# Optimization experiments

Measured on AMD Instinct MI355X. Metric: run time of the kernel, lower is better.

Reference implementation:

```python
import jax, jax.numpy as jnp
import numpy as np

HEADS = 20
HEAD_DIM = 64
NUM_IP = 20          # num_content_tokens (4) + num_style_tokens (16)
FU_SCALE = 0.5
STYLE_SCALE = 1.0
SCALE = 1.0 / np.sqrt(HEAD_DIM).astype(np.float32)


def setup_inputs() -> dict:
    key = jax.random.key(0)
    ks = jax.random.split(key, 9)
    B, S, H, C = 4, 4096, 1280, 2048
    T = 77 + NUM_IP  # text tokens + ip tokens
    w = 0.02
    return {
        "hidden_states": jax.random.normal(ks[0], (B, S, H), jnp.float32),
        "encoder_hidden_states": jax.random.normal(ks[1], (B, T, C), jnp.float32),
        "Wq": jax.random.normal(ks[2], (H, H), jnp.float32) * w,
        "Wk": jax.random.normal(ks[3], (H, C), jnp.float32) * w,
        "Wv": jax.random.normal(ks[4], (H, C), jnp.float32) * w,
        "Wk_ip": jax.random.normal(ks[5], (H, C), jnp.float32) * w,
        "Wv_ip": jax.random.normal(ks[6], (H, C), jnp.float32) * w,
        "Wo": jax.random.normal(ks[7], (H, H), jnp.float32) * w,
        "bo": jnp.zeros((H,), jnp.float32),
    }


def _to_heads(x):
    # [B, T, H] -> [B, heads, T, head_dim]
    B, T, _ = x.shape
    return x.reshape(B, T, HEADS, HEAD_DIM).transpose(0, 2, 1, 3)


def _blend(p):
    # cross-batch prob fusion: rows 1<-0, 3<-2 (CFG pairs)
    p = p.at[1].set(FU_SCALE * p[1] + (1.0 - FU_SCALE) * p[0])
    p = p.at[3].set(FU_SCALE * p[3] + (1.0 - FU_SCALE) * p[2])
    return p


def reference(hidden_states, encoder_hidden_states, Wq, Wk, Wv, Wk_ip, Wv_ip, Wo, bo):
    B, S, H = hidden_states.shape
    text = encoder_hidden_states[:, :-NUM_IP, :]   # [B, 77, C]
    ip = encoder_hidden_states[:, -NUM_IP:, :]     # [B, 20, C]

    q = _to_heads(hidden_states @ Wq.T)            # [B, h, S, d]
    k = _to_heads(text @ Wk.T)                     # [B, h, 77, d]
    v = _to_heads(text @ Wv.T)

    # fuAttn branch: explicit probs, blended across batch, then PV matmul
    probs = jax.nn.softmax(jnp.einsum('bhqd,bhkd->bhqk', q, k) * SCALE, axis=-1)
    probs = _blend(probs)
    raw = jnp.einsum('bhqk,bhkd->bhqd', probs, v)
    raw = raw.transpose(0, 2, 1, 3).reshape(B, S, H)

    # IP-adapter style cross-attention (fuIPAttn branch)
    ip_k = _to_heads(ip @ Wk_ip.T)                 # [B, h, 20, d]
    ip_v = _to_heads(ip @ Wv_ip.T)
    ip_probs = jax.nn.softmax(jnp.einsum('bhqd,bhkd->bhqk', q, ip_k) * SCALE, axis=-1)
    ip_probs = _blend(ip_probs)
    ip_hs = jnp.einsum('bhqk,bhkd->bhqd', ip_probs, ip_v)
    ip_hs = ip_hs.transpose(0, 2, 1, 3).reshape(B, S, H)

    hs = raw + STYLE_SCALE * ip_hs
    # batch rows 0 and 2 keep raw (text-only) attention output
    hs = hs.at[0].set(raw[0]).at[2].set(raw[2])

    # to_out[0] linear (bias) + to_out[1] dropout (identity at inference)
    return hs @ Wo.T + bo
```

## Files before the change

kernel.cpp:

```cpp
#include <hip/hip_runtime.h>
#include <cstdint>

typedef float floatx4 __attribute__((ext_vector_type(4)));
typedef __bf16 bf16x8 __attribute__((ext_vector_type(8)));

typedef const __attribute__((address_space(1))) void* gas_cvp;
typedef __attribute__((address_space(3))) void* las_vp;

__device__ __forceinline__ float bflo(unsigned int u) {
    return __builtin_bit_cast(float, u << 16);
}
__device__ __forceinline__ float bfhi(unsigned int u) {
    return __builtin_bit_cast(float, u & 0xffff0000u);
}
__device__ __forceinline__ unsigned short f2bf(float f) {
    unsigned int u = __builtin_bit_cast(unsigned int, f);
    u += 0x7fffu + ((u >> 16) & 1u);
    return (unsigned short)(u >> 16);
}
__device__ __forceinline__ bf16x8 ld8(const unsigned short* p) {
    return __builtin_bit_cast(bf16x8, *(const uint4*)p);
}
__device__ __forceinline__ floatx4 mfma32(bf16x8 a, bf16x8 b, floatx4 c) {
    return __builtin_amdgcn_mfma_f32_16x16x32_bf16(a, b, c, 0, 0, 0);
}
__device__ __forceinline__ void load_lds16(const void* g, void* l) {
    __builtin_amdgcn_global_load_lds(
        (gas_cvp)(unsigned long long)g,
        (las_vp)(unsigned int)(unsigned long long)l,
        16, 0, 0);
}

__global__ void cvt_f32_bf16(const float* __restrict__ in,
                             unsigned short* __restrict__ out, int n4) {
    int i = blockIdx.x * 256 + threadIdx.x;
    if (i < n4) {
        float4 v = ((const float4*)in)[i];
        ushort4 o;
        o.x = f2bf(v.x); o.y = f2bf(v.y); o.z = f2bf(v.z); o.w = f2bf(v.w);
        ((ushort4*)out)[i] = o;
    }
}

struct CvtJob { const float* src; unsigned short* dst; int n4; };
struct CvtJobs { CvtJob j[6]; };

__global__ void cvt_multi(CvtJobs jobs) {
    CvtJob jb = jobs.j[blockIdx.y];
    int i = blockIdx.x * 256 + threadIdx.x;
    if (i < jb.n4) {
        float4 v = ((const float4*)jb.src)[i];
        ushort4 o;
        o.x = f2bf(v.x); o.y = f2bf(v.y); o.z = f2bf(v.z); o.w = f2bf(v.w);
        ((ushort4*)jb.dst)[i] = o;
    }
}

__global__ void cvt_ehs(const float* __restrict__ ehs,
                        unsigned short* __restrict__ text,
                        unsigned short* __restrict__ ip) {
    int i = blockIdx.x * 256 + threadIdx.x;
    if (i < 384 * 512) {
        int r = i >> 9, c = i & 511;
        int b = r / 96, t = r - b * 96;
        ushort4 o = {0, 0, 0, 0};
        if (t < 77) {
            float4 v = *(const float4*)&ehs[((size_t)(b * 97 + t)) * 2048 + c * 4];
            o.x = f2bf(v.x); o.y = f2bf(v.y); o.z = f2bf(v.z); o.w = f2bf(v.w);
        }
        ((ushort4*)text)[i] = o;
    } else {
        int i2 = i - 384 * 512;
        if (i2 < 128 * 512) {
            int r = i2 >> 9, c = i2 & 511;
            int b = r >> 5, t = r & 31;
            ushort4 o = {0, 0, 0, 0};
            if (t < 20) {
                float4 v = *(const float4*)&ehs[((size_t)(b * 97 + 77 + t)) * 2048 + c * 4];
                o.x = f2bf(v.x); o.y = f2bf(v.y); o.z = f2bf(v.z); o.w = f2bf(v.w);
            }
            ((ushort4*)ip)[i2] = o;
        }
    }
}

struct GJob {
    const unsigned short* A;
    const unsigned short* B;
    void* C;
    int M, K;
    int Bn;
    int nt;
    int ldc;
    int bstart;
};
struct GArgs { GJob j[5]; };

template <bool F32OUT>
__global__ __launch_bounds__(512, 2) void gemm256(GArgs args,
                                                  const float* __restrict__ bias) {
    const int tid = threadIdx.x;
    int jid = 0;
#pragma unroll
    for (int t = 1; t < 5; ++t)
        if ((int)blockIdx.x >= args.j[t].bstart) jid = t;
    const GJob jb = args.j[jid];
    const int K = jb.K;
    int b = (int)blockIdx.x - jb.bstart;
    {
        const int mt = (jb.M + 255) >> 8;
        const int nblk = mt * jb.nt;
        if ((nblk & 7) == 0) b = (b & 7) * (nblk >> 3) + (b >> 3);
    }
    const int by = b / jb.nt, bx = b - by * jb.nt;

    __shared__ unsigned short ldsA[32768];
    __shared__ unsigned short ldsB[32768];

    const int srow   = ((tid >> 7) << 4) + ((tid >> 2) & 15);
    const int schunk = ((tid & 3) << 4) ^ (((tid >> 2) & 6) << 3);
    const int scol   = (((tid >> 6) & 1) << 5) + (schunk >> 1);

    const int Mloc = jb.M, BnL = jb.Bn;

    const unsigned short* pA[2][2];
    const unsigned short* pB[2][2];
    unsigned short* dA[2][2];
    unsigned short* dB[2][2];
#pragma unroll
    for (int h = 0; h < 2; ++h)
#pragma unroll
        for (int j = 0; j < 2; ++j) {
            const int r = h * 128 + j * 64 + srow;
            int ra = by * 256 + r;  ra = (ra < Mloc) ? ra : (Mloc - 1);
            int rb2 = bx * 256 + r; rb2 = (rb2 < BnL) ? rb2 : (BnL - 1);
            pA[h][j] = jb.A + (size_t)ra * K + scol;
            pB[h][j] = jb.B + (size_t)rb2 * K + scol;
            dA[h][j] = &ldsA[h * 8192 + j * 4096 + tid * 8];
            dB[h][j] = &ldsB[h * 8192 + j * 4096 + tid * 8];
        }

    const int lane = tid & 63, fr = lane & 15, g = lane >> 4;
    const int w = tid >> 6, wr = w & 1, wc = w >> 1;
    const int rb   = fr * 32 + ((g * 8) ^ ((fr & 6) << 2));
    const int aoff = wr * 8192 + rb;
    const int boff = (wc >> 1) * 8192 + (wc & 1) * 4096 + rb;

    floatx4 acc[8][4] = {};

    const int KT = K >> 6;

#pragma unroll
    for (int h = 0; h < 2; ++h)
#pragma unroll
        for (int j = 0; j < 2; ++j) {
            load_lds16(pA[h][j], dA[h][j]);
            load_lds16(pB[h][j], dB[h][j]);
        }
    asm volatile("s_waitcnt vmcnt(0)" ::: "memory");
    __builtin_amdgcn_s_barrier();

    for (int u = 0; u < KT; ++u) {
        const int pb = (u & 1) << 14;
        const int qb = pb ^ 16384;
        const int k1 = (u + 1 < KT) ? (u + 1) : (KT - 1);

#pragma unroll
        for (int h = 0; h < 2; ++h)
#pragma unroll
            for (int j = 0; j < 2; ++j) {
                load_lds16(pA[h][j] + (size_t)k1 * 64, dA[h][j] + qb);
                load_lds16(pB[h][j] + (size_t)k1 * 64, dB[h][j] + qb);
            }
        __builtin_amdgcn_sched_barrier(0);

#pragma unroll
        for (int kk = 0; kk < 2; ++kk) {
            bf16x8 af[8], bfr[4];
#pragma unroll
            for (int mi = 0; mi < 8; ++mi)
                af[mi] = *(const bf16x8*)&ldsA[pb + aoff + (mi * 2 + kk) * 512];
#pragma unroll
            for (int nf = 0; nf < 4; ++nf)
                bfr[nf] = *(const bf16x8*)&ldsB[pb + boff + (nf * 2 + kk) * 512];
            __builtin_amdgcn_s_setprio(1);
#pragma unroll
            for (int mi = 0; mi < 8; ++mi)
#pragma unroll
                for (int nf = 0; nf < 4; ++nf)
                    acc[mi][nf] = mfma32(af[mi], bfr[nf], acc[mi][nf]);
            __builtin_amdgcn_s_setprio(0);
        }

        asm volatile("s_waitcnt vmcnt(0)" ::: "memory");
        __builtin_amdgcn_s_barrier();
    }

    const int colBase = bx * 256 + wc * 64;
    const int rowBase = by * 256 + wr * 128;
    const int ldc = jb.ldc;
    float bv[4] = {};
    if (F32OUT) {
#pragma unroll
        for (int nf = 0; nf < 4; ++nf) bv[nf] = bias[colBase + nf * 16 + fr];
    }
#pragma unroll
    for (int mi = 0; mi < 8; ++mi) {
#pragma unroll
        for (int nf = 0; nf < 4; ++nf) {
            const int col  = colBase + nf * 16 + fr;
            const int row0 = rowBase + mi * 16 + g * 4;
#pragma unroll
            for (int r = 0; r < 4; ++r) {
                const int row = row0 + r;
                if (row < Mloc) {
                    float v = acc[mi][nf][r];
                    if (F32OUT)
                        ((float*)jb.C)[(size_t)row * ldc + col] = v + bv[nf];
                    else
                        ((unsigned short*)jb.C)[(size_t)row * ldc + col] = f2bf(v);
                }
            }
        }
    }
}

#define NT 77
#define NI 20

__global__ __launch_bounds__(256, 4) void attn_mfma(
    const unsigned short* __restrict__ q,
    const unsigned short* __restrict__ kt,
    const unsigned short* __restrict__ vtT,
    const unsigned short* __restrict__ kip,
    const unsigned short* __restrict__ ipT,
    unsigned short* __restrict__ outp)
{
    const int tid = threadIdx.x;
    const int qt = blockIdx.x;
    const int h  = blockIdx.y;
    const int pz = blockIdx.z;
    const int b0 = 2 * pz;
    const int lane  = tid & 63;
    const int w     = tid >> 6;
    const int bi    = w >> 1;
    const int strip = (w & 1) * 16;
    const int fr = lane & 15;
    const int g  = lane >> 4;

    __shared__ unsigned short sP[2][32][104];

    for (int i = tid; i < 2 * 32 * 24; i += 256) {
        int b = i / (32 * 24); int rem = i % (32 * 24);
        sP[b][rem / 24][80 + rem % 24] = 0;
    }

    const size_t qbase = ((size_t)((b0 + bi) * 4096 + qt * 32 + strip + fr)) * 1280 + h * 64;
    bf16x8 aq0 = ld8(&q[qbase + g * 8]);
    bf16x8 aq1 = ld8(&q[qbase + 32 + g * 8]);

    floatx4 sc[5] = {};
#pragma unroll
    for (int t = 0; t < 5; t++) {
        int key = t * 16 + fr;
        const size_t kb = ((size_t)((b0 + bi) * 96 + key)) * 1280 + h * 64;
        sc[t] = mfma32(aq0, ld8(&kt[kb + g * 8]), sc[t]);
        sc[t] = mfma32(aq1, ld8(&kt[kb + 32 + g * 8]), sc[t]);
    }

#pragma unroll
    for (int r = 0; r < 4; r++) {
        float m = -1e30f;
#pragma unroll
        for (int t = 0; t < 5; t++) {
            float v = sc[t][r] * 0.125f;
            if (t == 4 && fr >= 13) v = -1e30f;
            sc[t][r] = v;
            m = fmaxf(m, v);
        }
        m = fmaxf(m, __shfl_xor(m, 1));
        m = fmaxf(m, __shfl_xor(m, 2));
        m = fmaxf(m, __shfl_xor(m, 4));
        m = fmaxf(m, __shfl_xor(m, 8));
        float sum = 0.f;
#pragma unroll
        for (int t = 0; t < 5; t++) {
            float e = __expf(sc[t][r] - m);
            sc[t][r] = e;
            sum += e;
        }
        sum += __shfl_xor(sum, 1);
        sum += __shfl_xor(sum, 2);
        sum += __shfl_xor(sum, 4);
        sum += __shfl_xor(sum, 8);
        float inv = 1.f / sum;
#pragma unroll
        for (int t = 0; t < 5; t++)
            sP[bi][strip + g * 4 + r][t * 16 + fr] = f2bf(sc[t][r] * inv);
    }
    __syncthreads();

    {
        unsigned int* p0 = (unsigned int*)&sP[0][0][0];
        unsigned int* p1 = (unsigned int*)&sP[1][0][0];
        for (int i = tid; i < 32 * 104 / 2; i += 256) {
            unsigned int a = p0[i], b = p1[i];
            unsigned short r0 = f2bf(0.5f * (bflo(a) + bflo(b)));
            unsigned short r1 = f2bf(0.5f * (bfhi(a) + bfhi(b)));
            p1[i] = (unsigned int)r0 | ((unsigned int)r1 << 16);
        }
    }
    __syncthreads();

    floatx4 accO[4] = {};
    {
        const unsigned short* prow = &sP[bi][strip + fr][0];
        bf16x8 pa0 = ld8(prow + g * 8);
        bf16x8 pa1 = ld8(prow + 32 + g * 8);
        bf16x8 pa2 = ld8(prow + 64 + g * 8);
        const int vcol = (b0 + bi) * 96;
#pragma unroll
        for (int dt = 0; dt < 4; dt++) {
            const unsigned short* vrow = &vtT[(size_t)(h * 64 + dt * 16 + fr) * 512 + vcol];
            accO[dt] = mfma32(pa0, ld8(vrow + g * 8), accO[dt]);
            accO[dt] = mfma32(pa1, ld8(vrow + 32 + g * 8), accO[dt]);
            accO[dt] = mfma32(pa2, ld8(vrow + 64 + g * 8), accO[dt]);
        }
    }

    floatx4 si[2] = {};
#pragma unroll
    for (int t = 0; t < 2; t++) {
        int key = t * 16 + fr;
        const size_t kb = ((size_t)((b0 + bi) * 32 + key)) * 1280 + h * 64;
        si[t] = mfma32(aq0, ld8(&kip[kb + g * 8]), si[t]);
        si[t] = mfma32(aq1, ld8(&kip[kb + 32 + g * 8]), si[t]);
    }
#pragma unroll
    for (int r = 0; r < 4; r++) {
        float v0 = si[0][r] * 0.125f;
        float v1 = (fr >= 4) ? -1e30f : si[1][r] * 0.125f;
        float m = fmaxf(v0, v1);
        m = fmaxf(m, __shfl_xor(m, 1));
        m = fmaxf(m, __shfl_xor(m, 2));
        m = fmaxf(m, __shfl_xor(m, 4));
        m = fmaxf(m, __shfl_xor(m, 8));
        float e0 = __expf(v0 - m), e1 = __expf(v1 - m);
        float s = e0 + e1;
        s += __shfl_xor(s, 1);
        s += __shfl_xor(s, 2);
        s += __shfl_xor(s, 4);
        s += __shfl_xor(s, 8);
        float inv = 1.f / s;
        si[0][r] = e0 * inv;
        si[1][r] = e1 * inv;
    }
    __syncthreads();

#pragma unroll
    for (int r = 0; r < 4; r++) {
        sP[bi][strip + g * 4 + r][fr]      = f2bf(si[0][r]);
        sP[bi][strip + g * 4 + r][16 + fr] = f2bf(si[1][r]);
    }
    __syncthreads();

    for (int i = tid; i < 32 * 16; i += 256) {
        int r = i >> 4, kk = i & 15;
        unsigned int* p0 = (unsigned int*)&sP[0][r][0];
        unsigned int* p1 = (unsigned int*)&sP[1][r][0];
        unsigned int a = p0[kk], b = p1[kk];
        unsigned short r0 = f2bf(0.5f * (bflo(a) + bflo(b)));
        unsigned short r1 = f2bf(0.5f * (bfhi(a) + bfhi(b)));
        p1[kk] = (unsigned int)r0 | ((unsigned int)r1 << 16);
    }
    __syncthreads();

    if (bi == 1) {
        const unsigned short* prow = &sP[1][strip + fr][0];
        bf16x8 pip = ld8(prow + g * 8);
        const int icol = (b0 + 1) * 32;
#pragma unroll
        for (int dt = 0; dt < 4; dt++)
            accO[dt] = mfma32(pip,
                              ld8(&ipT[(size_t)(h * 64 + dt * 16 + fr) * 256 + icol + g * 8]),
                              accO[dt]);
    }

    const size_t orow0 = (size_t)((b0 + bi) * 4096 + qt * 32 + strip);
#pragma unroll
    for (int dt = 0; dt < 4; dt++) {
        int col = h * 64 + dt * 16 + fr;
#pragma unroll
        for (int r = 0; r < 4; r++)
            outp[(orow0 + g * 4 + r) * 1280 + col] = f2bf(accO[dt][r]);
    }
}

extern "C" void kernel_launch(void* const* d_in, const int* in_sizes, int n_in,
                              void* d_out, int out_size, void* d_ws, size_t ws_size,
                              hipStream_t stream) {
    const float* hs   = (const float*)d_in[0];
    const float* ehs  = (const float*)d_in[1];
    const float* Wq   = (const float*)d_in[2];
    const float* Wk   = (const float*)d_in[3];
    const float* Wv   = (const float*)d_in[4];
    const float* Wkip = (const float*)d_in[5];
    const float* Wvip = (const float*)d_in[6];
    const float* Wo   = (const float*)d_in[7];
    const float* bo   = (const float*)d_in[8];

    char* w = (char*)d_ws;
    size_t off = 0;
    auto alloc = [&](size_t bytes) {
        char* pp = w + off;
        off += (bytes + 255) & ~(size_t)255;
        return pp;
    };
    unsigned short* hs_bf   = (unsigned short*)alloc(16384ull * 1280 * 2);
    unsigned short* q_bf    = (unsigned short*)alloc(16384ull * 1280 * 2);
    unsigned short* at_bf   = (unsigned short*)alloc(16384ull * 1280 * 2);
    unsigned short* text_pad= (unsigned short*)alloc(384ull * 2048 * 2);
    unsigned short* ip_pad  = (unsigned short*)alloc(128ull * 2048 * 2);
    unsigned short* Wq_bf   = (unsigned short*)alloc(1280ull * 1280 * 2);
    unsigned short* Wk_bf   = (unsigned short*)alloc(1280ull * 2048 * 2);
    unsigned short* Wv_bf   = (unsigned short*)alloc(1280ull * 2048 * 2);
    unsigned short* Wkip_bf = (unsigned short*)alloc(1280ull * 2048 * 2);
    unsigned short* Wvip_bf = (unsigned short*)alloc(1280ull * 2048 * 2);
    unsigned short* Wo_bf   = (unsigned short*)alloc(1280ull * 1280 * 2);
    unsigned short* kt  = (unsigned short*)alloc(384ull * 1280 * 2);
    unsigned short* vtT = (unsigned short*)alloc(1280ull * 512 * 2);
    unsigned short* kip = (unsigned short*)alloc(128ull * 1280 * 2);
    unsigned short* ipT = (unsigned short*)alloc(1280ull * 256 * 2);

    cvt_f32_bf16<<<dim3(20480, 1, 1), 256, 0, stream>>>(hs, hs_bf, 16384 * 1280 / 4);

    cvt_ehs<<<dim3(1024, 1, 1), 256, 0, stream>>>(ehs, text_pad, ip_pad);

    CvtJobs cj{};
    cj.j[0] = CvtJob{Wq,   Wq_bf,   1280 * 1280 / 4};
    cj.j[1] = CvtJob{Wk,   Wk_bf,   1280 * 2048 / 4};
    cj.j[2] = CvtJob{Wv,   Wv_bf,   1280 * 2048 / 4};
    cj.j[3] = CvtJob{Wkip, Wkip_bf, 1280 * 2048 / 4};
    cj.j[4] = CvtJob{Wvip, Wvip_bf, 1280 * 2048 / 4};
    cj.j[5] = CvtJob{Wo,   Wo_bf,   1280 * 1280 / 4};
    cvt_multi<<<dim3(2560, 6, 1), 256, 0, stream>>>(cj);

    GArgs g1{};
    g1.j[0] = GJob{text_pad, Wk_bf,   (void*)kt,    384, 2048, 1280, 5, 1280,  0};
    g1.j[1] = GJob{ip_pad,   Wkip_bf, (void*)kip,   128, 2048, 1280, 5, 1280, 10};
    g1.j[2] = GJob{Wv_bf,    text_pad,(void*)vtT,  1280, 2048,  384, 2,  512, 15};
    g1.j[3] = GJob{Wvip_bf,  ip_pad,  (void*)ipT,  1280, 2048,  128, 1,  256, 25};
    g1.j[4] = GJob{hs_bf,    Wq_bf,   (void*)q_bf,16384, 1280, 1280, 5, 1280, 30};
    gemm256<false><<<dim3(350, 1, 1), 512, 0, stream>>>(g1, nullptr);

    attn_mfma<<<dim3(128, 20, 2), 256, 0, stream>>>(q_bf, kt, vtT, kip, ipT, at_bf);

    GArgs g2{};
    g2.j[0] = GJob{at_bf, Wo_bf, d_out, 16384, 1280, 1280, 5, 1280, 0};
    for (int t = 1; t < 5; ++t) g2.j[t].bstart = 0x7fffffff;
    gemm256<true><<<dim3(320, 1, 1), 512, 0, stream>>>(g2, bo);
}
```

Baseline: 439.6 us.

## Restructure GEMM mainloop into four-slot K32 ring buffer with staggered wave order

Replaces the double-buffered K=64 tile pipeline with a four-slot ring of K=32 stages, loading two stages ahead and synchronizing once per pair of stages. The LDS layout and swizzle are redone for 32-wide rows, and half the waves process the two resident stages in swapped order to spread LDS bank and port pressure. The aim is fewer barriers per unit of K and deeper prefetch. The cost is more complex indexing, and K must be a multiple of 64 for the pair loop to cover every stage.

Result: slower. 452.1 us (+2.9%).

```diff
diff --git a/kernel.cpp b/kernel.cpp
--- a/kernel.cpp
+++ b/kernel.cpp
@@ -114,87 +114,74 @@
     }
     const int by = b / jb.nt, bx = b - by * jb.nt;
 
-    __shared__ unsigned short ldsA[32768];
-    __shared__ unsigned short ldsB[32768];
-
-    const int srow   = ((tid >> 7) << 4) + ((tid >> 2) & 15);
-    const int schunk = ((tid & 3) << 4) ^ (((tid >> 2) & 6) << 3);
-    const int scol   = (((tid >> 6) & 1) << 5) + (schunk >> 1);
+    __shared__ unsigned short lds[4][16384];
+
+    const int srow = tid >> 2;
+    const int scol = (((tid & 3) ^ ((tid >> 3) & 3)) << 3);
 
     const int Mloc = jb.M, BnL = jb.Bn;
-
-    const unsigned short* pA[2][2];
-    const unsigned short* pB[2][2];
-    unsigned short* dA[2][2];
-    unsigned short* dB[2][2];
-#pragma unroll
-    for (int h = 0; h < 2; ++h)
-#pragma unroll
-        for (int j = 0; j < 2; ++j) {
-            const int r = h * 128 + j * 64 + srow;
-            int ra = by * 256 + r;  ra = (ra < Mloc) ? ra : (Mloc - 1);
-            int rb2 = bx * 256 + r; rb2 = (rb2 < BnL) ? rb2 : (BnL - 1);
-            pA[h][j] = jb.A + (size_t)ra * K + scol;
-            pB[h][j] = jb.B + (size_t)rb2 * K + scol;
-            dA[h][j] = &ldsA[h * 8192 + j * 4096 + tid * 8];
-            dB[h][j] = &ldsB[h * 8192 + j * 4096 + tid * 8];
-        }
+    int ra0 = by * 256 + srow;        ra0 = (ra0 < Mloc) ? ra0 : (Mloc - 1);
+    int ra1 = by * 256 + 128 + srow;  ra1 = (ra1 < Mloc) ? ra1 : (Mloc - 1);
+    int rb0 = bx * 256 + srow;        rb0 = (rb0 < BnL) ? rb0 : (BnL - 1);
+    int rb1 = bx * 256 + 128 + srow;  rb1 = (rb1 < BnL) ? rb1 : (BnL - 1);
+    const unsigned short* pa0 = jb.A + (size_t)ra0 * K + scol;
+    const unsigned short* pa1 = jb.A + (size_t)ra1 * K + scol;
+    const unsigned short* pb0 = jb.B + (size_t)rb0 * K + scol;
+    const unsigned short* pb1 = jb.B + (size_t)rb1 * K + scol;
 
     const int lane = tid & 63, fr = lane & 15, g = lane >> 4;
     const int w = tid >> 6, wr = w & 1, wc = w >> 1;
-    const int rb   = fr * 32 + ((g * 8) ^ ((fr & 6) << 2));
-    const int aoff = wr * 8192 + rb;
-    const int boff = (wc >> 1) * 8192 + (wc & 1) * 4096 + rb;
+    const int rswz  = ((g ^ ((fr >> 1) & 3)) << 3);
+    const int abase = (wr * 128 + fr) * 32 + rswz;
+    const int bbase = 8192 + (wc * 64 + fr) * 32 + rswz;
+    const int ord   = (w >> 2) & 1;
 
     floatx4 acc[8][4] = {};
 
-    const int KT = K >> 6;
-
-#pragma unroll
-    for (int h = 0; h < 2; ++h)
-#pragma unroll
-        for (int j = 0; j < 2; ++j) {
-            load_lds16(pA[h][j], dA[h][j]);
-            load_lds16(pB[h][j], dB[h][j]);
-        }
-    asm volatile("s_waitcnt vmcnt(0)" ::: "memory");
-    __builtin_amdgcn_s_barrier();
-
-    for (int u = 0; u < KT; ++u) {
-        const int pb = (u & 1) << 14;
-        const int qb = pb ^ 16384;
-        const int k1 = (u + 1 < KT) ? (u + 1) : (KT - 1);
-
-#pragma unroll
-        for (int h = 0; h < 2; ++h)
-#pragma unroll
-            for (int j = 0; j < 2; ++j) {
-                load_lds16(pA[h][j] + (size_t)k1 * 64, dA[h][j] + qb);
-                load_lds16(pB[h][j] + (size_t)k1 * 64, dB[h][j] + qb);
-            }
-        __builtin_amdgcn_sched_barrier(0);
-
-#pragma unroll
-        for (int kk = 0; kk < 2; ++kk) {
-            bf16x8 af[8], bfr[4];
-#pragma unroll
-            for (int mi = 0; mi < 8; ++mi)
-                af[mi] = *(const bf16x8*)&ldsA[pb + aoff + (mi * 2 + kk) * 512];
-#pragma unroll
-            for (int nf = 0; nf < 4; ++nf)
-                bfr[nf] = *(const bf16x8*)&ldsB[pb + boff + (nf * 2 + kk) * 512];
-            __builtin_amdgcn_s_setprio(1);
-#pragma unroll
-            for (int mi = 0; mi < 8; ++mi)
-#pragma unroll
-                for (int nf = 0; nf < 4; ++nf)
-                    acc[mi][nf] = mfma32(af[mi], bfr[nf], acc[mi][nf]);
-            __builtin_amdgcn_s_setprio(0);
-        }
-
+    const int NS = K >> 5;
+    const int NP = NS >> 1;
+
+    auto stage = [&](int s, int slot) {
+        const size_t k0 = (size_t)s << 5;
+        unsigned short* base = &lds[slot][0];
+        load_lds16(pa0 + k0, base + tid * 8);
+        load_lds16(pa1 + k0, base + 4096 + tid * 8);
+        load_lds16(pb0 + k0, base + 8192 + tid * 8);
+        load_lds16(pb1 + k0, base + 12288 + tid * 8);
+    };
+
+    stage(0, 0);
+    stage(1, 1);
+
+    for (int P = 0; P < NP; ++P) {
         asm volatile("s_waitcnt vmcnt(0)" ::: "memory");
         __builtin_amdgcn_s_barrier();
-    }
+
+        int s2 = 2 * P + 2, s3 = 2 * P + 3;
+        stage((s2 < NS) ? s2 : (NS - 1), s2 & 3);
+        stage((s3 < NS) ? s3 : (NS - 1), s3 & 3);
+        __builtin_amdgcn_sched_barrier(0);
+
+#pragma unroll
+        for (int hh = 0; hh < 2; ++hh) {
+            const unsigned short* sl = &lds[(2 * P + (hh ^ ord)) & 3][0];
+            bf16x8 af[8], bf[4];
+#pragma unroll
+            for (int mi = 0; mi < 8; ++mi)
+                af[mi] = *(const bf16x8*)&sl[abase + mi * 512];
+#pragma unroll
+            for (int nf = 0; nf < 4; ++nf)
+                bf[nf] = *(const bf16x8*)&sl[bbase + nf * 512];
+            __builtin_amdgcn_s_setprio(1);
+#pragma unroll
+            for (int mi = 0; mi < 8; ++mi)
+#pragma unroll
+                for (int nf = 0; nf < 4; ++nf)
+                    acc[mi][nf] = mfma32(af[mi], bf[nf], acc[mi][nf]);
+            __builtin_amdgcn_s_setprio(0);
+        }
+    }
+    asm volatile("s_waitcnt vmcnt(0)" ::: "memory");
 
     const int colBase = bx * 256 + wc * 64;
     const int rowBase = by * 256 + wr * 128;
```
